# Kernel tuning notes

Measured on AMD Instinct MI355X. Metric: run time of the kernel, lower is better.

Reference implementation:

```python
import jax, jax.numpy as jnp
import numpy as np

NUM_CLASSES = 80
MASK_SIZE = 3
MAX_BOXES = 50
NET_W = 608.0
NET_H = 608.0
ANCHORS = np.array([10.,13.,16.,30.,33.,23.,30.,61.,62.,45.,59.,119.,116.,90.,156.,198.,373.,326.], dtype=np.float32).reshape(9, 2)


def setup_inputs():
    key = jax.random.key(0)
    k1, k2, k3 = jax.random.split(key, 3)
    B, H, W = 16, 76, 76
    inp = jax.random.normal(k1, (B, MASK_SIZE * (5 + NUM_CLASSES), H, W), dtype=jnp.float32) * 0.5
    cls = jax.random.randint(k2, (B, MAX_BOXES, 1), 0, NUM_CLASSES).astype(jnp.float32)
    coords = jax.random.uniform(k3, (B, MAX_BOXES, 4), minval=0.02, maxval=0.95, dtype=jnp.float32)
    targets = jnp.concatenate([cls, coords], axis=-1).reshape(B, MAX_BOXES * 5)
    return {"input": inp, "targets": targets}


def _forward(inp, targets):
    B, _, H, W = inp.shape
    A, C = MASK_SIZE, NUM_CLASSES
    anchors = jnp.asarray(ANCHORS)  # [9,2]; masked anchor inds are [0,1,2]
    pred = inp.reshape(B, A, 5 + C, H, W).transpose(0, 1, 3, 4, 2)  # [B,A,H,W,5+C]
    x = jax.nn.sigmoid(pred[..., 0])
    y = jax.nn.sigmoid(pred[..., 1])
    w = pred[..., 2]
    h = pred[..., 3]
    conf = jax.nn.sigmoid(pred[..., 4])
    pred_cls = jax.nn.sigmoid(pred[..., 5:])

    tg = targets.reshape(B, -1, 5)  # [B,T,5] = (cls, x, y, w, h) normalized
    valid = jnp.sum(tg, axis=-1) != 0  # [B,T]
    tcls, tx, ty, tw, th = (tg[..., i] for i in range(5))
    gi = jnp.clip((tx * W).astype(jnp.int32), 0, W - 1)
    gj = jnp.clip((ty * H).astype(jnp.int32), 0, H - 1)

    # best of all 9 anchors via zero-centered IoU (boxes share center -> inter = min(w)*min(h))
    aw = anchors[:, 0] / NET_W
    ah = anchors[:, 1] / NET_H
    inter = jnp.minimum(tw[..., None], aw) * jnp.minimum(th[..., None], ah)
    union = tw[..., None] * th[..., None] + aw * ah - inter
    best_anchor = jnp.argmax(inter / union, axis=-1)  # [B,T]
    assigned = valid & (best_anchor < A)  # masked_anchor_inds == [0..A-1]
    wgt = assigned.astype(jnp.float32)
    a_n = best_anchor % A
    aw_s = anchors[a_n, 0]
    ah_s = anchors[a_n, 1]

    tx_t = tx * W - gi.astype(jnp.float32)
    ty_t = ty * H - gj.astype(jnp.float32)
    tw_safe = jnp.where(assigned, tw, 1.0)
    th_safe = jnp.where(assigned, th, 1.0)
    tw_t = jnp.log(tw_safe * NET_W / aw_s)
    th_t = jnp.log(th_safe * NET_H / ah_s)
    scale = 2.0 * ty * tw  # faithful to original: 2 * t[2] * t[3]

    bidx = jnp.arange(B)[:, None]
    px = x[bidx, a_n, gj, gi]
    py = y[bidx, a_n, gj, gi]
    pw = w[bidx, a_n, gj, gi]
    ph = h[bidx, a_n, gj, gi]
    pconf = conf[bidx, a_n, gj, gi]
    pcls = pred_cls[bidx, a_n, gj, gi]  # [B,T,C]

    loss_x = jnp.sum(wgt * scale * jnp.abs(px - tx_t))
    loss_y = jnp.sum(wgt * scale * jnp.abs(py - ty_t))
    loss_w = jnp.sum(wgt * scale * jnp.abs(pw - tw_t))
    loss_h = jnp.sum(wgt * scale * jnp.abs(ph - th_t))

    one_hot = jax.nn.one_hot(tcls.astype(jnp.int32), C, dtype=jnp.float32)
    bce = -(one_hot * jnp.log(pcls) + (1.0 - one_hot) * jnp.log1p(-pcls))
    loss_cls = jnp.sum(wgt[..., None] * bce)

    num_truths = jnp.maximum(jnp.sum(valid.astype(jnp.float32)), 1.0)

    # loss_objectness = -conf everywhere; assigned cells overwritten with (1 - conf)
    loss_obj = (-conf).reshape(-1)
    flat_idx = ((bidx * A + a_n) * H + gj) * W + gi  # [B,T]
    flat_idx = jnp.where(assigned, flat_idx, loss_obj.size)  # OOB -> dropped
    loss_obj = loss_obj.at[flat_idx.reshape(-1)].set((1.0 - pconf).reshape(-1), mode='drop')
    return -jnp.sum(loss_obj) + (loss_x + loss_y + loss_w + loss_h) / num_truths + loss_cls


def reference(input, targets):
    return _forward(input, targets)
```

## Files before the change

kernel.cpp:

```cpp
#include <hip/hip_runtime.h>

constexpr int B_  = 16;
constexpr int A_  = 3;
constexpr int C_  = 80;
constexpr int T_  = 50;
constexpr int H_  = 76;
constexpr int W_  = 76;
constexpr int HW_ = H_ * W_;
constexpr int BSTR_ = A_ * (5 + C_) * HW_;
constexpr float NETW_ = 608.0f;
constexpr float NETH_ = 608.0f;

constexpr int NCONF_BLOCKS  = 192;
constexpr int CONF_SLICES   = B_ * A_;
constexpr int F4_PER_SLICE  = HW_ / 4;
constexpr int CONF_F4       = CONF_SLICES * F4_PER_SLICE;

__device__ const float ANCH[18] = {
    10.f, 13.f, 16.f, 30.f, 33.f, 23.f, 30.f, 61.f, 62.f,
    45.f, 59.f, 119.f, 116.f, 90.f, 156.f, 198.f, 373.f, 326.f};

__device__ __forceinline__ float sigf(float z) {
    return 1.0f / (1.0f + expf(-z));
}

__device__ __forceinline__ float waveRed(float v) {
    #pragma unroll
    for (int o = 32; o > 0; o >>= 1) v += __shfl_down(v, o);
    return v;
}

__global__ __launch_bounds__(256) void yolo_main(const float* __restrict__ inp,
                                                 const float* __restrict__ tgt,
                                                 float* __restrict__ ws) {
    const int tid = threadIdx.x;
    const int bid = blockIdx.x;

    if (bid >= B_) {
        const int cb = bid - B_;
        float s = 0.0f;
        for (int f = cb * 256 + tid; f < CONF_F4; f += NCONF_BLOCKS * 256) {
            const int sl   = f / F4_PER_SLICE;
            const int pos4 = f - sl * F4_PER_SLICE;
            const int b    = sl / A_;
            const int a    = sl - b * A_;
            const float4 v = *reinterpret_cast<const float4*>(
                inp + b * BSTR_ + (a * 85 + 4) * HW_ + pos4 * 4);
            s += sigf(v.x) + sigf(v.y) + sigf(v.z) + sigf(v.w);
        }
        __shared__ float red[4];
        s = waveRed(s);
        if ((tid & 63) == 0) red[tid >> 6] = s;
        __syncthreads();
        if (tid == 0) ws[64 + cb] = red[0] + red[1] + red[2] + red[3];
        return;
    }

    const int b = bid;
    __shared__ int sh_cell[T_];
    __shared__ int sh_base[T_];
    __shared__ int sh_cls[T_];

    float lcoord = 0.0f, lcls = 0.0f, vcnt = 0.0f, ucnt = 0.0f;

    if (tid < T_) sh_cell[tid] = -1;

    if (tid < T_) {
        const float* tp = tgt + (b * T_ + tid) * 5;
        const float tc = tp[0], tx = tp[1], ty = tp[2], tw = tp[3], th = tp[4];
        const bool valid = (tc + tx + ty + tw + th) != 0.0f;
        vcnt = valid ? 1.0f : 0.0f;

        float bestv = -1.0f;
        int besti = 0;
        #pragma unroll
        for (int k = 0; k < 9; ++k) {
            const float aw = ANCH[2 * k]     * (1.0f / NETW_);
            const float ah = ANCH[2 * k + 1] * (1.0f / NETH_);
            const float in = fminf(tw, aw) * fminf(th, ah);
            const float un = tw * th + aw * ah - in;
            const float iou = in / un;
            if (iou > bestv) { bestv = iou; besti = k; }
        }

        if (valid && besti < A_) {
            int gi = (int)(tx * (float)W_);
            gi = gi < 0 ? 0 : (gi > W_ - 1 ? W_ - 1 : gi);
            int gj = (int)(ty * (float)H_);
            gj = gj < 0 ? 0 : (gj > H_ - 1 ? H_ - 1 : gj);

            const int cell = (besti * H_ + gj) * W_ + gi;
            const int base = b * BSTR_ + besti * 85 * HW_ + gj * W_ + gi;
            sh_cell[tid] = cell;
            sh_base[tid] = base;
            sh_cls[tid]  = (int)tc;

            const float txt = tx * (float)W_ - (float)gi;
            const float tyt = ty * (float)H_ - (float)gj;
            const float twt = logf(tw * NETW_ / ANCH[2 * besti]);
            const float tht = logf(th * NETH_ / ANCH[2 * besti + 1]);
            const float scale = 2.0f * ty * tw;

            const float px = sigf(inp[base]);
            const float py = sigf(inp[base + HW_]);
            const float pw = inp[base + 2 * HW_];
            const float ph = inp[base + 3 * HW_];
            lcoord = scale * (fabsf(px - txt) + fabsf(py - tyt) +
                              fabsf(pw - twt) + fabsf(ph - tht));
        }
    }
    __syncthreads();

    if (tid < T_ && sh_cell[tid] >= 0) {
        bool uniq = true;
        for (int q = 0; q < tid; ++q)
            if (sh_cell[q] == sh_cell[tid]) { uniq = false; break; }
        ucnt = uniq ? 1.0f : 0.0f;
    }

    for (int p = tid; p < T_ * C_; p += 256) {
        const int t = p / C_;
        const int c = p - t * C_;
        if (sh_cell[t] >= 0) {
            const float z  = inp[sh_base[t] + (5 + c) * HW_];
            const float pc = sigf(z);
            const float oh = (c == sh_cls[t]) ? 1.0f : 0.0f;
            lcls -= oh * logf(pc) + (1.0f - oh) * log1pf(-pc);
        }
    }

    __shared__ float red2[4][4];
    float vals[4] = {lcoord, lcls, vcnt, ucnt};
    #pragma unroll
    for (int k = 0; k < 4; ++k) {
        const float r = waveRed(vals[k]);
        if ((tid & 63) == 0) red2[k][tid >> 6] = r;
    }
    __syncthreads();
    if (tid == 0) {
        ws[b]      = red2[0][0] + red2[0][1] + red2[0][2] + red2[0][3];
        ws[16 + b] = red2[1][0] + red2[1][1] + red2[1][2] + red2[1][3];
        ws[32 + b] = red2[2][0] + red2[2][1] + red2[2][2] + red2[2][3];
        ws[48 + b] = red2[3][0] + red2[3][1] + red2[3][2] + red2[3][3];
    }
}

__global__ __launch_bounds__(256) void yolo_fin(const float* __restrict__ ws,
                                                float* __restrict__ out) {
    const int tid = threadIdx.x;
    float s = 0.0f;
    for (int i = tid; i < NCONF_BLOCKS; i += 256) s += ws[64 + i];
    __shared__ float red[4];
    s = waveRed(s);
    if ((tid & 63) == 0) red[tid >> 6] = s;
    __syncthreads();
    if (tid == 0) {
        const float conf_sum = red[0] + red[1] + red[2] + red[3];
        float lcoord = 0.f, lcls = 0.f, vcnt = 0.f, ucnt = 0.f;
        for (int b = 0; b < B_; ++b) {
            lcoord += ws[b];
            lcls   += ws[16 + b];
            vcnt   += ws[32 + b];
            ucnt   += ws[48 + b];
        }
        const float nt = fmaxf(vcnt, 1.0f);
        out[0] = (conf_sum - ucnt) + lcoord / nt + lcls;
    }
}

extern "C" void kernel_launch(void* const* d_in, const int* in_sizes, int n_in,
                              void* d_out, int out_size, void* d_ws, size_t ws_size,
                              hipStream_t stream) {
    const float* inp = (const float*)d_in[0];
    const float* tgt = (const float*)d_in[1];
    float* ws  = (float*)d_ws;
    float* out = (float*)d_out;

    yolo_main<<<B_ + NCONF_BLOCKS, 256, 0, stream>>>(inp, tgt, ws);
    yolo_fin<<<1, 256, 0, stream>>>(ws, out);
}
```

Before: 123.5 us.

## Spread class BCE gathers across all blocks and merge with the confidence sum

The per-class BCE work used to run on only 16 per-batch blocks. It is now distributed over a grid-stride loop across all 256 blocks, and each thread recomputes its target's anchor assignment instead of reading it from shared memory. BCE and confidence terms share one accumulator and one reduction slot per block. The coordinate, valid-count and unique-cell terms stay on the first 16 blocks. This removes the serial gather-latency tail on those 16 blocks, at the cost of redundant per-thread target loads and IoU arithmetic.

```diff
diff --git a/kernel.cpp b/kernel.cpp
--- a/kernel.cpp
+++ b/kernel.cpp
@@ -11,10 +11,10 @@
 constexpr float NETW_ = 608.0f;
 constexpr float NETH_ = 608.0f;
 
-constexpr int NCONF_BLOCKS  = 192;
-constexpr int CONF_SLICES   = B_ * A_;
-constexpr int F4_PER_SLICE  = HW_ / 4;
-constexpr int CONF_F4       = CONF_SLICES * F4_PER_SLICE;
+constexpr int NB_          = 256;
+constexpr int F4_PER_SLICE = HW_ / 4;
+constexpr int CONF_F4      = B_ * A_ * F4_PER_SLICE;
+constexpr int NBCE_        = B_ * T_ * C_;
 
 __device__ const float ANCH[18] = {
     10.f, 13.f, 16.f, 30.f, 33.f, 23.f, 30.f, 61.f, 62.f,
@@ -30,118 +30,120 @@
     return v;
 }
 
+__device__ __forceinline__ bool assign_target(const float* __restrict__ tgt,
+                                              int b, int t,
+                                              float& tc, float& tx, float& ty,
+                                              float& tw, float& th,
+                                              int& besti, int& gi, int& gj) {
+    const float* tp = tgt + (b * T_ + t) * 5;
+    tc = tp[0]; tx = tp[1]; ty = tp[2]; tw = tp[3]; th = tp[4];
+    const bool valid = (tc + tx + ty + tw + th) != 0.0f;
+
+    float bestv = -1.0f;
+    besti = 0;
+    #pragma unroll
+    for (int k = 0; k < 9; ++k) {
+        const float aw = ANCH[2 * k]     * (1.0f / NETW_);
+        const float ah = ANCH[2 * k + 1] * (1.0f / NETH_);
+        const float in = fminf(tw, aw) * fminf(th, ah);
+        const float un = tw * th + aw * ah - in;
+        const float iou = in / un;
+        if (iou > bestv) { bestv = iou; besti = k; }
+    }
+    if (!(valid && besti < A_)) return false;
+
+    gi = (int)(tx * (float)W_);
+    gi = gi < 0 ? 0 : (gi > W_ - 1 ? W_ - 1 : gi);
+    gj = (int)(ty * (float)H_);
+    gj = gj < 0 ? 0 : (gj > H_ - 1 ? H_ - 1 : gj);
+    return true;
+}
+
 __global__ __launch_bounds__(256) void yolo_main(const float* __restrict__ inp,
                                                  const float* __restrict__ tgt,
                                                  float* __restrict__ ws) {
     const int tid = threadIdx.x;
     const int bid = blockIdx.x;
+    const int gt  = bid * 256 + tid;
+    constexpr int GT = NB_ * 256;
 
-    if (bid >= B_) {
-        const int cb = bid - B_;
-        float s = 0.0f;
-        for (int f = cb * 256 + tid; f < CONF_F4; f += NCONF_BLOCKS * 256) {
-            const int sl   = f / F4_PER_SLICE;
-            const int pos4 = f - sl * F4_PER_SLICE;
-            const int b    = sl / A_;
-            const int a    = sl - b * A_;
-            const float4 v = *reinterpret_cast<const float4*>(
-                inp + b * BSTR_ + (a * 85 + 4) * HW_ + pos4 * 4);
-            s += sigf(v.x) + sigf(v.y) + sigf(v.z) + sigf(v.w);
-        }
-        __shared__ float red[4];
-        s = waveRed(s);
-        if ((tid & 63) == 0) red[tid >> 6] = s;
-        __syncthreads();
-        if (tid == 0) ws[64 + cb] = red[0] + red[1] + red[2] + red[3];
-        return;
+    float acc = 0.0f;
+
+    for (int f = gt; f < CONF_F4; f += GT) {
+        const int sl   = f / F4_PER_SLICE;
+        const int pos4 = f - sl * F4_PER_SLICE;
+        const int b    = sl / A_;
+        const int a    = sl - b * A_;
+        const float4 v = *reinterpret_cast<const float4*>(
+            inp + b * BSTR_ + (a * 85 + 4) * HW_ + pos4 * 4);
+        acc += sigf(v.x) + sigf(v.y) + sigf(v.z) + sigf(v.w);
     }
 
-    const int b = bid;
-    __shared__ int sh_cell[T_];
-    __shared__ int sh_base[T_];
-    __shared__ int sh_cls[T_];
-
-    float lcoord = 0.0f, lcls = 0.0f, vcnt = 0.0f, ucnt = 0.0f;
-
-    if (tid < T_) sh_cell[tid] = -1;
-
-    if (tid < T_) {
-        const float* tp = tgt + (b * T_ + tid) * 5;
-        const float tc = tp[0], tx = tp[1], ty = tp[2], tw = tp[3], th = tp[4];
-        const bool valid = (tc + tx + ty + tw + th) != 0.0f;
-        vcnt = valid ? 1.0f : 0.0f;
-
-        float bestv = -1.0f;
-        int besti = 0;
-        #pragma unroll
-        for (int k = 0; k < 9; ++k) {
-            const float aw = ANCH[2 * k]     * (1.0f / NETW_);
-            const float ah = ANCH[2 * k + 1] * (1.0f / NETH_);
-            const float in = fminf(tw, aw) * fminf(th, ah);
-            const float un = tw * th + aw * ah - in;
-            const float iou = in / un;
-            if (iou > bestv) { bestv = iou; besti = k; }
-        }
-
-        if (valid && besti < A_) {
-            int gi = (int)(tx * (float)W_);
-            gi = gi < 0 ? 0 : (gi > W_ - 1 ? W_ - 1 : gi);
-            int gj = (int)(ty * (float)H_);
-            gj = gj < 0 ? 0 : (gj > H_ - 1 ? H_ - 1 : gj);
-
-            const int cell = (besti * H_ + gj) * W_ + gi;
+    for (int p = gt; p < NBCE_; p += GT) {
+        const int b = p / (T_ * C_);
+        const int r = p - b * (T_ * C_);
+        const int t = r / C_;
+        const int c = r - t * C_;
+        float tc, tx, ty, tw, th;
+        int besti, gi, gj;
+        if (assign_target(tgt, b, t, tc, tx, ty, tw, th, besti, gi, gj)) {
             const int base = b * BSTR_ + besti * 85 * HW_ + gj * W_ + gi;
-            sh_cell[tid] = cell;
-            sh_base[tid] = base;
-            sh_cls[tid]  = (int)tc;
-
-            const float txt = tx * (float)W_ - (float)gi;
-            const float tyt = ty * (float)H_ - (float)gj;
-            const float twt = logf(tw * NETW_ / ANCH[2 * besti]);
-            const float tht = logf(th * NETH_ / ANCH[2 * besti + 1]);
-            const float scale = 2.0f * ty * tw;
-
-            const float px = sigf(inp[base]);
-            const float py = sigf(inp[base + HW_]);
-            const float pw = inp[base + 2 * HW_];
-            const float ph = inp[base + 3 * HW_];
-            lcoord = scale * (fabsf(px - txt) + fabsf(py - tyt) +
-                              fabsf(pw - twt) + fabsf(ph - tht));
-        }
-    }
-    __syncthreads();
-
-    if (tid < T_ && sh_cell[tid] >= 0) {
-        bool uniq = true;
-        for (int q = 0; q < tid; ++q)
-            if (sh_cell[q] == sh_cell[tid]) { uniq = false; break; }
-        ucnt = uniq ? 1.0f : 0.0f;
-    }
-
-    for (int p = tid; p < T_ * C_; p += 256) {
-        const int t = p / C_;
-        const int c = p - t * C_;
-        if (sh_cell[t] >= 0) {
-            const float z  = inp[sh_base[t] + (5 + c) * HW_];
-            const float pc = sigf(z);
-            const float oh = (c == sh_cls[t]) ? 1.0f : 0.0f;
-            lcls -= oh * logf(pc) + (1.0f - oh) * log1pf(-pc);
+            const float pc = sigf(inp[base + (5 + c) * HW_]);
+            const float oh = (c == (int)tc) ? 1.0f : 0.0f;
+            acc -= oh * logf(pc) + (1.0f - oh) * log1pf(-pc);
         }
     }
 
-    __shared__ float red2[4][4];
-    float vals[4] = {lcoord, lcls, vcnt, ucnt};
-    #pragma unroll
-    for (int k = 0; k < 4; ++k) {
-        const float r = waveRed(vals[k]);
-        if ((tid & 63) == 0) red2[k][tid >> 6] = r;
+    __shared__ int sh_cell[T_];
+    float lcoord = 0.0f, vcnt = 0.0f, ucnt = 0.0f;
+    if (bid < B_) {
+        if (tid < T_) sh_cell[tid] = -1;
+        if (tid < T_) {
+            float tc, tx, ty, tw, th;
+            int besti, gi, gj;
+            const float* tp = tgt + (bid * T_ + tid) * 5;
+            const float sum5 = tp[0] + tp[1] + tp[2] + tp[3] + tp[4];
+            vcnt = (sum5 != 0.0f) ? 1.0f : 0.0f;
+            if (assign_target(tgt, bid, tid, tc, tx, ty, tw, th, besti, gi, gj)) {
+                sh_cell[tid] = (besti * H_ + gj) * W_ + gi;
+                const int base = bid * BSTR_ + besti * 85 * HW_ + gj * W_ + gi;
+                const float txt = tx * (float)W_ - (float)gi;
+                const float tyt = ty * (float)H_ - (float)gj;
+                const float twt = logf(tw * NETW_ / ANCH[2 * besti]);
+                const float tht = logf(th * NETH_ / ANCH[2 * besti + 1]);
+                const float scale = 2.0f * ty * tw;
+                const float px = sigf(inp[base]);
+                const float py = sigf(inp[base + HW_]);
+                const float pw = inp[base + 2 * HW_];
+                const float ph = inp[base + 3 * HW_];
+                lcoord = scale * (fabsf(px - txt) + fabsf(py - tyt) +
+                                  fabsf(pw - twt) + fabsf(ph - tht));
+            }
+        }
+        __syncthreads();
+        if (tid < T_ && sh_cell[tid] >= 0) {
+            bool uniq = true;
+            for (int q = 0; q < tid; ++q)
+                if (sh_cell[q] == sh_cell[tid]) { uniq = false; break; }
+            ucnt = uniq ? 1.0f : 0.0f;
+        }
     }
+
+    __shared__ float red[4];
+    const float r = waveRed(acc);
+    if ((tid & 63) == 0) red[tid >> 6] = r;
     __syncthreads();
-    if (tid == 0) {
-        ws[b]      = red2[0][0] + red2[0][1] + red2[0][2] + red2[0][3];
-        ws[16 + b] = red2[1][0] + red2[1][1] + red2[1][2] + red2[1][3];
-        ws[32 + b] = red2[2][0] + red2[2][1] + red2[2][2] + red2[2][3];
-        ws[48 + b] = red2[3][0] + red2[3][1] + red2[3][2] + red2[3][3];
+    if (tid == 0) ws[64 + bid] = red[0] + red[1] + red[2] + red[3];
+
+    if (bid < B_) {
+        const float lr = waveRed(lcoord);
+        const float vr = waveRed(vcnt);
+        const float ur = waveRed(ucnt);
+        if (tid == 0) {
+            ws[bid]      = lr;
+            ws[32 + bid] = vr;
+            ws[48 + bid] = ur;
+        }
     }
 }
 
@@ -149,22 +151,21 @@
                                                 float* __restrict__ out) {
     const int tid = threadIdx.x;
     float s = 0.0f;
-    for (int i = tid; i < NCONF_BLOCKS; i += 256) s += ws[64 + i];
+    for (int i = tid; i < NB_; i += 256) s += ws[64 + i];
     __shared__ float red[4];
-    s = waveRed(s);
-    if ((tid & 63) == 0) red[tid >> 6] = s;
+    const float r = waveRed(s);
+    if ((tid & 63) == 0) red[tid >> 6] = r;
     __syncthreads();
     if (tid == 0) {
-        const float conf_sum = red[0] + red[1] + red[2] + red[3];
-        float lcoord = 0.f, lcls = 0.f, vcnt = 0.f, ucnt = 0.f;
+        const float conf_bce = red[0] + red[1] + red[2] + red[3];
+        float lcoord = 0.f, vcnt = 0.f, ucnt = 0.f;
         for (int b = 0; b < B_; ++b) {
             lcoord += ws[b];
-            lcls   += ws[16 + b];
             vcnt   += ws[32 + b];
             ucnt   += ws[48 + b];
         }
         const float nt = fmaxf(vcnt, 1.0f);
-        out[0] = (conf_sum - ucnt) + lcoord / nt + lcls;
+        out[0] = (conf_bce - ucnt) + lcoord / nt;
     }
 }
 
@@ -176,6 +177,6 @@
     float* ws  = (float*)d_ws;
     float* out = (float*)d_out;
 
-    yolo_main<<<B_ + NCONF_BLOCKS, 256, 0, stream>>>(inp, tgt, ws);
+    yolo_main<<<NB_, 256, 0, stream>>>(inp, tgt, ws);
     yolo_fin<<<1, 256, 0, stream>>>(ws, out);
 }
```

Result: no change. 125.3 us (+1.5%).
